# Optimization experiments

Measured on AMD Instinct MI355X. Metric: run time of the kernel, lower is better.

Reference implementation:

```python
import jax, jax.numpy as jnp
import numpy as np

N_NODES = 100000
N_EDGES = 1600000
D_IN = 128
D_OUT = 128


def setup_inputs() -> dict:
    key = jax.random.key(0)
    k1, k2, k3 = jax.random.split(key, 3)
    x = jax.random.normal(k1, (N_NODES, D_IN), dtype=jnp.float32)
    edge_index = jax.random.randint(k2, (2, N_EDGES), 0, N_NODES, dtype=jnp.int64)
    # Glorot-style init for the GCN weight, zero bias (PyG defaults)
    W = jax.random.normal(k3, (D_IN, D_OUT), dtype=jnp.float32) * (1.0 / np.sqrt(D_IN))
    b = jnp.zeros((D_OUT,), dtype=jnp.float32)
    return {"x": x, "edge_index": edge_index, "W": W, "b": b}


def reference(x, edge_index, W, b):
    # GCNConv (PyG defaults: add_self_loops=True, normalize=True):
    #   out = D^{-1/2} (A + I) D^{-1/2} (X W) + b
    # Dropout is identity in eval mode.
    n = x.shape[0]
    loop = jnp.arange(n, dtype=edge_index.dtype)
    src = jnp.concatenate([edge_index[0], loop])  # [E + N]
    dst = jnp.concatenate([edge_index[1], loop])  # [E + N]

    h = x @ W  # [N, D_OUT] -- transform before aggregation (fewer FLOPs if D_OUT <= D_IN)

    # Degree of each node counting self-loops, computed over targets.
    ones = jnp.ones(dst.shape[0], dtype=h.dtype)
    deg = jax.ops.segment_sum(ones, dst, num_segments=n)  # [N]
    deg_inv_sqrt = jnp.where(deg > 0, jax.lax.rsqrt(deg), 0.0)

    # Symmetric normalization per edge: d_src^{-1/2} * d_dst^{-1/2}
    norm = deg_inv_sqrt[src] * deg_inv_sqrt[dst]  # [E + N]

    # Gather messages, scale, scatter-add to targets.
    msgs = h[src] * norm[:, None]  # [E + N, D_OUT]
    out = jax.ops.segment_sum(msgs, dst, num_segments=n)  # [N, D_OUT]
    return out + b
```

## Files before the change

kernel.cpp:

```cpp
#include <hip/hip_runtime.h>

#define DD 128
#define CAP 12288

typedef __attribute__((ext_vector_type(8))) short bf16x8;
typedef __attribute__((ext_vector_type(4))) float f32x4;

__device__ inline unsigned short f2b(float f) {
    unsigned int u = __float_as_uint(f);
    u += 0x7fffu + ((u >> 16) & 1u);
    return (unsigned short)(u >> 16);
}

__device__ inline void bacc(float4& a, uint2 v) {
    a.x += __uint_as_float(v.x << 16);
    a.y += __uint_as_float(v.x & 0xffff0000u);
    a.z += __uint_as_float(v.y << 16);
    a.w += __uint_as_float(v.y & 0xffff0000u);
}

__device__ inline void bacc16(float4& a, float4& b, uint4 v) {
    a.x += __uint_as_float(v.x << 16);
    a.y += __uint_as_float(v.x & 0xffff0000u);
    a.z += __uint_as_float(v.y << 16);
    a.w += __uint_as_float(v.y & 0xffff0000u);
    b.x += __uint_as_float(v.z << 16);
    b.y += __uint_as_float(v.z & 0xffff0000u);
    b.z += __uint_as_float(v.w << 16);
    b.w += __uint_as_float(v.w & 0xffff0000u);
}

__global__ void k_init(int* __restrict__ cur, int nbuck) {
    int b = blockIdx.x * 256 + threadIdx.x;
    if (b < nbuck) cur[b] = b * CAP;
}

__global__ __launch_bounds__(256) void k_binA(const int* __restrict__ src,
                                              const int* __restrict__ dst, int E,
                                              int chunk, int nbuck,
                                              int* __restrict__ cur,
                                              int* __restrict__ binned) {
    __shared__ int hist[256];
    __shared__ int base[256];
    __shared__ int curs[256];
    const int t = threadIdx.x;
    const int e0 = blockIdx.x * chunk;
    const int e1 = min(e0 + chunk, E);

    if (t < 256) { hist[t] = 0; curs[t] = 0; }
    __syncthreads();
    for (int e = e0 + t; e < e1; e += 256)
        atomicAdd(&hist[dst[e] >> 9], 1);
    __syncthreads();
    if (t < nbuck && hist[t] > 0)
        base[t] = atomicAdd(&cur[t], hist[t]);
    __syncthreads();
    for (int e = e0 + t; e < e1; e += 256) {
        int d = dst[e];
        int b = d >> 9;
        int p = atomicAdd(&curs[b], 1);
        int idx = base[b] + p;
        if (idx < (b + 1) * CAP)
            binned[idx] = (src[e] << 9) | (d & 511);
    }
}

__global__ __launch_bounds__(512) void k_binB(int* __restrict__ binned,
                                              const int* __restrict__ cur,
                                              int* __restrict__ off,
                                              int* __restrict__ cnt,
                                              float* __restrict__ dinv,
                                              int n) {
    __shared__ int hist[512];
    __shared__ int curs[512];
    __shared__ int sorted[CAP];
    const int t = threadIdx.x;
    const int b = blockIdx.x;
    const int base = b * CAP;
    const int cb = cur[b] - base;

    hist[t] = 0;
    __syncthreads();
    for (int i = t; i < cb; i += 512)
        atomicAdd(&hist[binned[base + i] & 511], 1);
    __syncthreads();
    int v = hist[t];
    for (int st = 1; st < 512; st <<= 1) {
        int tv = (t >= st) ? hist[t - st] : 0;
        __syncthreads();
        hist[t] += tv;
        __syncthreads();
    }
    int excl = hist[t] - v;
    curs[t] = excl;
    int d = b * 512 + t;
    if (d < n) {
        off[d]  = base + excl;
        cnt[d]  = v;
        dinv[d] = rsqrtf((float)v + 1.0f);
    }
    __syncthreads();
    for (int i = t; i < cb; i += 512) {
        int pk = binned[base + i];
        int p = atomicAdd(&curs[pk & 511], 1);
        sorted[p] = pk >> 9;
    }
    __syncthreads();
    for (int i = t; i < cb; i += 512)
        binned[base + i] = sorted[i];
}

__global__ __launch_bounds__(256) void k_wt(const float* __restrict__ W,
                                            unsigned short* __restrict__ Wt) {
    int idx = blockIdx.x * 256 + threadIdx.x;
    int k = idx >> 7, c = idx & 127;
    Wt[c * DD + k] = f2b(W[k * DD + c]);
}

__global__ __launch_bounds__(256) void k_gemm(const float* __restrict__ x,
                                              const unsigned short* __restrict__ Wt,
                                              const float* __restrict__ dinv,
                                              unsigned short* __restrict__ hs,
                                              int n) {
    const int t = threadIdx.x;
    const int wave = t >> 6, lane = t & 63;
    const int rowbase = blockIdx.x * 256 + wave * 64;
    const int l15 = lane & 15, l4 = lane >> 4;

    bf16x8 a[4][4];
    #pragma unroll
    for (int rb = 0; rb < 4; ++rb) {
        int r = rowbase + rb * 16 + l15;
        int rc = min(r, n - 1);
        const float* xr = x + (size_t)rc * DD;
        #pragma unroll
        for (int kc = 0; kc < 4; ++kc) {
            int k0 = kc * 32 + l4 * 8;
            float4 f0 = *(const float4*)(xr + k0);
            float4 f1 = *(const float4*)(xr + k0 + 4);
            bf16x8 fr;
            fr[0] = (short)f2b(f0.x); fr[1] = (short)f2b(f0.y);
            fr[2] = (short)f2b(f0.z); fr[3] = (short)f2b(f0.w);
            fr[4] = (short)f2b(f1.x); fr[5] = (short)f2b(f1.y);
            fr[6] = (short)f2b(f1.z); fr[7] = (short)f2b(f1.w);
            a[rb][kc] = fr;
        }
    }

    float dv[4][4];
    #pragma unroll
    for (int rb = 0; rb < 4; ++rb)
        #pragma unroll
        for (int vv = 0; vv < 4; ++vv) {
            int r = rowbase + rb * 16 + l4 * 4 + vv;
            dv[rb][vv] = dinv[min(r, n - 1)];
        }

    #pragma unroll
    for (int cb = 0; cb < 8; ++cb) {
        int c0 = cb * 16;
        f32x4 acc[4] = {};
        #pragma unroll
        for (int kc = 0; kc < 4; ++kc) {
            bf16x8 bfrag = *(const bf16x8*)(Wt + (size_t)(c0 + l15) * DD + kc * 32 + l4 * 8);
            #pragma unroll
            for (int rb = 0; rb < 4; ++rb)
                acc[rb] = __builtin_amdgcn_mfma_f32_16x16x32_bf16(a[rb][kc], bfrag, acc[rb], 0, 0, 0);
        }
        #pragma unroll
        for (int rb = 0; rb < 4; ++rb) {
            int r0 = rowbase + rb * 16 + l4 * 4;
            #pragma unroll
            for (int vv = 0; vv < 4; ++vv) {
                int r = r0 + vv;
                if (r < n)
                    hs[(size_t)r * DD + c0 + l15] = f2b(acc[rb][vv] * dv[rb][vv]);
            }
        }
    }
}

__global__ __launch_bounds__(256, 8) void k_agg(const uint4* __restrict__ hsr,
                                                const int* __restrict__ ssrc,
                                                const int* __restrict__ off,
                                                const int* __restrict__ cnt,
                                                const float* __restrict__ dinv,
                                                const float* __restrict__ bias,
                                                float* __restrict__ out, int n) {
    const int t = threadIdx.x;
    const int wave = t >> 6, lane = t & 63;
    const int q  = lane >> 4;
    const int ql = lane & 15;
    const int d = blockIdx.x * 4 + wave;
    if (d >= n) return;

    const int s0 = off[d];
    const int c  = cnt[d];

    float4 accA = {0.f, 0.f, 0.f, 0.f};
    float4 accB = {0.f, 0.f, 0.f, 0.f};

    uint4 vself = hsr[(size_t)d * 16 + ql];

    int idx[6];
    #pragma unroll
    for (int r = 0; r < 6; ++r) {
        int e = r * 4 + q;
        idx[r] = ssrc[s0 + ((e < c) ? e : 0)];
    }
    #pragma unroll
    for (int r = 0; r < 6; ++r) {
        int e = r * 4 + q;
        idx[r] = (e < c) ? idx[r] : d;
    }

    uint4 val[6];
    #pragma unroll
    for (int r = 0; r < 6; ++r)
        val[r] = hsr[(size_t)idx[r] * 16 + ql];

    if (q == 0) bacc16(accA, accB, vself);
    #pragma unroll
    for (int r = 0; r < 6; ++r) {
        int e = r * 4 + q;
        if (e < c) bacc16(accA, accB, val[r]);
    }

    for (int i = 24 + q; i < c; i += 4) {
        int s = ssrc[s0 + i];
        uint4 v = hsr[(size_t)s * 16 + ql];
        bacc16(accA, accB, v);
    }

    #pragma unroll
    for (int m = 16; m <= 32; m <<= 1) {
        accA.x += __shfl_xor(accA.x, m);
        accA.y += __shfl_xor(accA.y, m);
        accA.z += __shfl_xor(accA.z, m);
        accA.w += __shfl_xor(accA.w, m);
        accB.x += __shfl_xor(accB.x, m);
        accB.y += __shfl_xor(accB.y, m);
        accB.z += __shfl_xor(accB.z, m);
        accB.w += __shfl_xor(accB.w, m);
    }

    if (q == 0) {
        float di = dinv[d];
        float4 b0 = ((const float4*)bias)[ql * 2];
        float4 b1 = ((const float4*)bias)[ql * 2 + 1];
        float4 o0, o1;
        o0.x = accA.x * di + b0.x;
        o0.y = accA.y * di + b0.y;
        o0.z = accA.z * di + b0.z;
        o0.w = accA.w * di + b0.w;
        o1.x = accB.x * di + b1.x;
        o1.y = accB.y * di + b1.y;
        o1.z = accB.z * di + b1.z;
        o1.w = accB.w * di + b1.w;
        float4* orow = (float4*)(out + (size_t)d * DD);
        orow[ql * 2]     = o0;
        orow[ql * 2 + 1] = o1;
    }
}

extern "C" void kernel_launch(void* const* d_in, const int* in_sizes, int n_in,
                              void* d_out, int out_size, void* d_ws, size_t ws_size,
                              hipStream_t stream) {
    const float* x  = (const float*)d_in[0];
    const int*   ei = (const int*)d_in[1];
    const float* W  = (const float*)d_in[2];
    const float* b  = (const float*)d_in[3];
    float* out = (float*)d_out;

    const int n = in_sizes[0] / DD;
    const int E = in_sizes[1] / 2;
    const int* src = ei;
    const int* dst = ei + E;

    const int nbuck = (n + 511) >> 9;

    unsigned short* hs = (unsigned short*)d_ws;
    unsigned short* Wt = hs + (size_t)n * DD;
    int*   binned = (int*)(Wt + DD * DD);
    int*   off    = binned + (size_t)nbuck * CAP;
    int*   cnt    = off + n;
    float* dinv   = (float*)(cnt + n);
    int*   cur    = (int*)(dinv + n);

    const int nblkA = 1024;
    const int chunk = (E + nblkA - 1) / nblkA;

    k_init<<<(nbuck + 255) / 256, 256, 0, stream>>>(cur, nbuck);
    k_binA<<<nblkA, 256, 0, stream>>>(src, dst, E, chunk, nbuck, cur, binned);
    k_binB<<<nbuck, 512, 0, stream>>>(binned, cur, off, cnt, dinv, n);
    k_wt  <<<DD * DD / 256, 256, 0, stream>>>(W, Wt);
    k_gemm<<<(n + 255) / 256, 256, 0, stream>>>(x, Wt, dinv, hs, n);
    k_agg <<<(n + 3) / 4, 256, 0, stream>>>((const uint4*)hs, binned, off, cnt,
                                            dinv, b, out, n);
}
```

Measured before the change: 136.9 us.

## Replace two-pass bucket sort with global-atomic CSR build fused into GEMM launch

Replaces the bucketed two-pass binning (coarse buckets then in-shared sort) with a degree count via global atomics, a wave-level scan with an atomic base, and an atomic scatter that builds the CSR. The Wt transpose is merged into the degree-count launch, and the scatter blocks share a launch with the GEMM blocks so the two run concurrently. The goal is fewer kernel launches, less staging traffic through the binned buffer, and overlap of edge scatter with the matmul. In exchange, CSR segments are no longer contiguous in node order (the scan is non-deterministic across waves) and neighbor order within a node is non-deterministic, and the global atomics can contend.

New measurement: 301.1 us. 2.2x slower.

```diff
diff --git a/kernel.cpp b/kernel.cpp
--- a/kernel.cpp
+++ b/kernel.cpp
@@ -1,7 +1,6 @@
 #include <hip/hip_runtime.h>
 
 #define DD 128
-#define CAP 12288
 
 typedef __attribute__((ext_vector_type(8))) short bf16x8;
 typedef __attribute__((ext_vector_type(4))) float f32x4;
@@ -10,13 +9,6 @@
     unsigned int u = __float_as_uint(f);
     u += 0x7fffu + ((u >> 16) & 1u);
     return (unsigned short)(u >> 16);
-}
-
-__device__ inline void bacc(float4& a, uint2 v) {
-    a.x += __uint_as_float(v.x << 16);
-    a.y += __uint_as_float(v.x & 0xffff0000u);
-    a.z += __uint_as_float(v.y << 16);
-    a.w += __uint_as_float(v.y & 0xffff0000u);
 }
 
 __device__ inline void bacc16(float4& a, float4& b, uint4 v) {
@@ -30,99 +22,67 @@
     b.w += __uint_as_float(v.w & 0xffff0000u);
 }
 
-__global__ void k_init(int* __restrict__ cur, int nbuck) {
-    int b = blockIdx.x * 256 + threadIdx.x;
-    if (b < nbuck) cur[b] = b * CAP;
-}
-
-__global__ __launch_bounds__(256) void k_binA(const int* __restrict__ src,
-                                              const int* __restrict__ dst, int E,
-                                              int chunk, int nbuck,
+__global__ __launch_bounds__(256) void k_pre(const float* __restrict__ W,
+                                             unsigned short* __restrict__ Wt,
+                                             const int* __restrict__ dst, int E,
+                                             int* __restrict__ deg) {
+    const int bid = blockIdx.x;
+    if (bid < 64) {
+        int idx = bid * 256 + threadIdx.x;
+        int k = idx >> 7, c = idx & 127;
+        Wt[c * DD + k] = f2b(W[k * DD + c]);
+    } else {
+        const int nb = gridDim.x - 64;
+        for (int e = (bid - 64) * 256 + threadIdx.x; e < E; e += nb * 256)
+            atomicAdd(&deg[dst[e]], 1);
+    }
+}
+
+__global__ __launch_bounds__(256) void k_scan(const int* __restrict__ deg,
+                                              int* __restrict__ off,
                                               int* __restrict__ cur,
-                                              int* __restrict__ binned) {
-    __shared__ int hist[256];
-    __shared__ int base[256];
-    __shared__ int curs[256];
-    const int t = threadIdx.x;
-    const int e0 = blockIdx.x * chunk;
-    const int e1 = min(e0 + chunk, E);
-
-    if (t < 256) { hist[t] = 0; curs[t] = 0; }
-    __syncthreads();
-    for (int e = e0 + t; e < e1; e += 256)
-        atomicAdd(&hist[dst[e] >> 9], 1);
-    __syncthreads();
-    if (t < nbuck && hist[t] > 0)
-        base[t] = atomicAdd(&cur[t], hist[t]);
-    __syncthreads();
-    for (int e = e0 + t; e < e1; e += 256) {
-        int d = dst[e];
-        int b = d >> 9;
-        int p = atomicAdd(&curs[b], 1);
-        int idx = base[b] + p;
-        if (idx < (b + 1) * CAP)
-            binned[idx] = (src[e] << 9) | (d & 511);
-    }
-}
-
-__global__ __launch_bounds__(512) void k_binB(int* __restrict__ binned,
-                                              const int* __restrict__ cur,
-                                              int* __restrict__ off,
-                                              int* __restrict__ cnt,
                                               float* __restrict__ dinv,
-                                              int n) {
-    __shared__ int hist[512];
-    __shared__ int curs[512];
-    __shared__ int sorted[CAP];
-    const int t = threadIdx.x;
-    const int b = blockIdx.x;
-    const int base = b * CAP;
-    const int cb = cur[b] - base;
-
-    hist[t] = 0;
-    __syncthreads();
-    for (int i = t; i < cb; i += 512)
-        atomicAdd(&hist[binned[base + i] & 511], 1);
-    __syncthreads();
-    int v = hist[t];
-    for (int st = 1; st < 512; st <<= 1) {
-        int tv = (t >= st) ? hist[t - st] : 0;
-        __syncthreads();
-        hist[t] += tv;
-        __syncthreads();
-    }
-    int excl = hist[t] - v;
-    curs[t] = excl;
-    int d = b * 512 + t;
+                                              int* __restrict__ gtot, int n) {
+    const int d = blockIdx.x * 256 + threadIdx.x;
+    const int lane = threadIdx.x & 63;
+    int orig = (d < n) ? deg[d] : 0;
+    int v = orig;
+    #pragma unroll
+    for (int m = 1; m < 64; m <<= 1) {
+        int up = __shfl_up(v, m);
+        if (lane >= m) v += up;
+    }
+    int base = 0;
+    if (lane == 63) base = atomicAdd(gtot, v);
+    base = __shfl(base, 63);
+    int excl = base + v - orig;
     if (d < n) {
-        off[d]  = base + excl;
-        cnt[d]  = v;
-        dinv[d] = rsqrtf((float)v + 1.0f);
-    }
-    __syncthreads();
-    for (int i = t; i < cb; i += 512) {
-        int pk = binned[base + i];
-        int p = atomicAdd(&curs[pk & 511], 1);
-        sorted[p] = pk >> 9;
-    }
-    __syncthreads();
-    for (int i = t; i < cb; i += 512)
-        binned[base + i] = sorted[i];
-}
-
-__global__ __launch_bounds__(256) void k_wt(const float* __restrict__ W,
-                                            unsigned short* __restrict__ Wt) {
-    int idx = blockIdx.x * 256 + threadIdx.x;
-    int k = idx >> 7, c = idx & 127;
-    Wt[c * DD + k] = f2b(W[k * DD + c]);
-}
-
-__global__ __launch_bounds__(256) void k_gemm(const float* __restrict__ x,
+        off[d]  = excl;
+        cur[d]  = excl;
+        dinv[d] = rsqrtf((float)orig + 1.0f);
+    }
+}
+
+__global__ __launch_bounds__(256) void k_work(const float* __restrict__ x,
                                               const unsigned short* __restrict__ Wt,
                                               const float* __restrict__ dinv,
                                               unsigned short* __restrict__ hs,
-                                              int n) {
+                                              const int* __restrict__ src,
+                                              const int* __restrict__ dst, int E,
+                                              int* __restrict__ cur,
+                                              int* __restrict__ csr,
+                                              int n, int ngemm) {
     const int t = threadIdx.x;
+    if ((int)blockIdx.x >= ngemm) {
+        const int nb = gridDim.x - ngemm;
+        for (int e = (blockIdx.x - ngemm) * 256 + t; e < E; e += nb * 256) {
+            int dd = dst[e];
+            int p = atomicAdd(&cur[dd], 1);
+            csr[p] = src[e];
+        }
+        return;
+    }
+
     const int wave = t >> 6, lane = t & 63;
     const int rowbase = blockIdx.x * 256 + wave * 64;
     const int l15 = lane & 15, l4 = lane >> 4;
@@ -277,24 +237,23 @@
     const int* src = ei;
     const int* dst = ei + E;
 
-    const int nbuck = (n + 511) >> 9;
-
     unsigned short* hs = (unsigned short*)d_ws;
     unsigned short* Wt = hs + (size_t)n * DD;
-    int*   binned = (int*)(Wt + DD * DD);
-    int*   off    = binned + (size_t)nbuck * CAP;
-    int*   cnt    = off + n;
-    float* dinv   = (float*)(cnt + n);
-    int*   cur    = (int*)(dinv + n);
-
-    const int nblkA = 1024;
-    const int chunk = (E + nblkA - 1) / nblkA;
-
-    k_init<<<(nbuck + 255) / 256, 256, 0, stream>>>(cur, nbuck);
-    k_binA<<<nblkA, 256, 0, stream>>>(src, dst, E, chunk, nbuck, cur, binned);
-    k_binB<<<nbuck, 512, 0, stream>>>(binned, cur, off, cnt, dinv, n);
-    k_wt  <<<DD * DD / 256, 256, 0, stream>>>(W, Wt);
-    k_gemm<<<(n + 255) / 256, 256, 0, stream>>>(x, Wt, dinv, hs, n);
-    k_agg <<<(n + 3) / 4, 256, 0, stream>>>((const uint4*)hs, binned, off, cnt,
+    int*   csr  = (int*)(Wt + DD * DD);
+    int*   off  = csr + E;
+    int*   cur  = off + n;
+    int*   deg  = cur + n;
+    int*   gtot = deg + n;
+    float* dinv = (float*)(gtot + 1);
+
+    hipMemsetAsync(deg, 0, (size_t)(n + 1) * sizeof(int), stream);
+
+    const int ngemm = (n + 255) / 256;
+
+    k_pre <<<64 + 1024, 256, 0, stream>>>(W, Wt, dst, E, deg);
+    k_scan<<<(n + 255) / 256, 256, 0, stream>>>(deg, off, cur, dinv, gtot, n);
+    k_work<<<ngemm + 1024, 256, 0, stream>>>(x, Wt, dinv, hs, src, dst, E,
+                                             cur, csr, n, ngemm);
+    k_agg <<<(n + 3) / 4, 256, 0, stream>>>((const uint4*)hs, csr, off, deg,
                                             dinv, b, out, n);
 }
```
